# Optimization experiments

Measured on AMD Instinct MI355X. Metric: run time of the kernel, lower is better.

Reference implementation:

```python
import jax, jax.numpy as jnp
import numpy as np

B, T, D, N, R = 2, 2048, 1024, 16, 64  # batch, seqlen, d_model, d_state, dt_rank


def setup_inputs() -> dict:
    key = jax.random.key(0)
    ks = jax.random.split(key, 8)
    sc = 0.02  # init scale for weights
    return {
        "x": jax.random.normal(ks[0], (B, T, D), jnp.float32),
        "W_in": jax.random.normal(ks[1], (2 * D, D), jnp.float32) * sc,   # in_proj.weight
        "conv_w": jax.random.normal(ks[2], (D, 3), jnp.float32) * sc,     # conv1d.weight [D,1,3] squeezed
        "W_x": jax.random.normal(ks[3], (R + 2 * N, D), jnp.float32) * sc, # x_proj.weight
        "W_dt": jax.random.normal(ks[4], (D, R), jnp.float32) * sc,        # dt_proj.weight
        "b_dt": jnp.ones((D,), jnp.float32),                               # dt_proj.bias (init 1.0)
        "A_log": jnp.full((D, N), -2.0, jnp.float32),                      # A_log (filled -2.0)
        "D_param": jnp.ones((D,), jnp.float32),                            # D skip
        "W_C": jax.random.normal(ks[5], (D, N), jnp.float32) * sc,         # C_proj.weight
        "W_out": jax.random.normal(ks[6], (D, D), jnp.float32) * sc,       # out_proj.weight
    }


def reference(x, W_in, conv_w, W_x, W_dt, b_dt, A_log, D_param, W_C, W_out):
    # in_proj -> chunk into (x, z)
    xz = jnp.einsum('btd,ed->bte', x, W_in)           # [B,T,2D]
    xc, z = jnp.split(xz, 2, axis=-1)                 # [B,T,D] each

    # depthwise conv1d, kernel 3, padding 1, no bias
    xp = jnp.pad(xc, ((0, 0), (1, 1), (0, 0)))
    xconv = (xp[:, :-2] * conv_w[:, 0]
             + xp[:, 1:-1] * conv_w[:, 1]
             + xp[:, 2:] * conv_w[:, 2])              # [B,T,D]
    xs = jax.nn.silu(xconv)

    # x_proj -> split dt / B / C params
    x_dbl = jnp.einsum('btd,ed->bte', xs, W_x)        # [B,T,R+2N]
    dt_param = x_dbl[..., :R]
    Bp = x_dbl[..., R:R + N]                          # [B,T,N]
    Cp = x_dbl[..., R + N:]                           # [B,T,N]

    dt = jax.nn.softplus(dt_param @ W_dt.T + b_dt) + 1e-5  # [B,T,D]

    # discretization
    A_disc = jnp.exp(-jnp.exp(A_log)[None, None] * dt[..., None])  # [B,T,D,N]
    Bx = Bp[:, :, None, :] * dt[..., None] * xs[..., None]         # [B,T,D,N]
    C = Cp @ W_C.T                                                  # [B,T,D]

    # selective scan: s_t = A_t * s_{t-1} + B_t * x_t;  y_t = C_t * sum_n s_t
    def step(s, inp):
        A_t, Bx_t = inp
        s = A_t * s + Bx_t
        return s, s.sum(-1)                           # carry [B,D,N], out [B,D]

    s0 = jnp.zeros((x.shape[0], D, N), x.dtype)
    _, ssum = jax.lax.scan(step, s0,
                           (A_disc.transpose(1, 0, 2, 3), Bx.transpose(1, 0, 2, 3)))
    ssum = ssum.transpose(1, 0, 2)                    # [B,T,D]

    y = C * ssum + D_param * xs                       # [B,T,D]
    return jnp.einsum('btd,ed->bte', y, W_out) * jax.nn.silu(z)
```

## Files before the change

### kernel.cpp

```cpp
#include <hip/hip_runtime.h>

typedef unsigned short u16;
typedef __attribute__((ext_vector_type(4))) float f4;
typedef __attribute__((ext_vector_type(4))) unsigned short us4;
typedef __attribute__((ext_vector_type(8))) unsigned short us8;
typedef __attribute__((ext_vector_type(8))) short s8v;
typedef __attribute__((ext_vector_type(4))) float f32x4;
typedef __attribute__((ext_vector_type(4))) unsigned int u4v;

#define DEVI __device__ __forceinline__

DEVI u16 f2bf(float f) {
  unsigned u = __float_as_uint(f);
  u = (u + 0x7FFFu + ((u >> 16) & 1u)) >> 16;
  return (u16)u;
}
DEVI float bf2f(u16 v) { return __uint_as_float(((unsigned)v) << 16); }
DEVI float siluf(float x) { return x / (1.f + __expf(-x)); }

__global__ void k_cvt_all(const float* __restrict__ x, const float* __restrict__ w1,
                          const float* __restrict__ wo, const float* __restrict__ wdt,
                          const float* __restrict__ wx,
                          u16* __restrict__ xb, u16* __restrict__ w1b,
                          u16* __restrict__ wob, u16* __restrict__ wdtb,
                          u16* __restrict__ wxb) {
  const int blk = blockIdx.x;
  const int tid = threadIdx.x;
  if (blk >= 7232) {
    int i = (blk - 7232) * 256 + tid;
    int row = i >> 8;
    us4 o;
    if (row < 96) {
      f4 v = ((const f4*)wx)[i];
#pragma unroll
      for (int j = 0; j < 4; ++j) o[j] = f2bf(v[j]);
    } else {
      o[0] = 0; o[1] = 0; o[2] = 0; o[3] = 0;
    }
    ((us4*)wxb)[i] = o;
    return;
  }
  const float* src; u16* dst; int i;
  if (blk < 4096)      { src = x;   dst = xb;   i = blk * 256 + tid; }
  else if (blk < 6144) { src = w1;  dst = w1b;  i = (blk - 4096) * 256 + tid; }
  else if (blk < 7168) { src = wo;  dst = wob;  i = (blk - 6144) * 256 + tid; }
  else                 { src = wdt; dst = wdtb; i = (blk - 7168) * 256 + tid; }
  f4 v = ((const f4*)src)[i];
  us4 o;
#pragma unroll
  for (int j = 0; j < 4; ++j) o[j] = f2bf(v[j]);
  ((us4*)dst)[i] = o;
}

template <int EPI>
__global__ __launch_bounds__(512, 2)
void k_gemm_bt(const u16* __restrict__ A, int lda,
               const u16* __restrict__ B, int ldb,
               float* __restrict__ C, int ldc, int nvalid,
               int K, int kchunk, size_t zstride, int lognx,
               const float* __restrict__ bvec,
               const u16* __restrict__ zsrc,
               u16* __restrict__ ob1, u16* __restrict__ ob2) {
  __shared__ __align__(16) char smem[16384];
  u16* As = (u16*)smem;
  u16* Bs = (u16*)(smem + 8192);
  const int tid = threadIdx.x;
  const int wave = tid >> 6, lane = tid & 63;

  const int nwg = gridDim.x * gridDim.y;
  int bid = blockIdx.y * gridDim.x + blockIdx.x;
  {
    const int cpx = nwg >> 3;
    bid = (bid & 7) * cpx + (bid >> 3);
  }
  const int mBase = (bid >> lognx) << 7;
  const int nBase = (bid & ((1 << lognx) - 1)) << 7;
  const int kbeg = blockIdx.z * kchunk;
  int kend = kbeg + kchunk; if (kend > K) kend = K;
  C += (size_t)blockIdx.z * zstride;

  const int wr = wave >> 2, wc = wave & 3;
  const int row0 = tid >> 2, kg = tid & 3;

  const u16* Ag = A + (size_t)(mBase + row0) * lda + kg * 8;
  const u16* Bg = B + (size_t)(nBase + row0) * ldb + kg * 8;
  char* ldsA = (char*)As + wave * 1024;
  char* ldsB = (char*)Bs + wave * 1024;

  const int fr = lane & 15, fk = (lane >> 4) << 3;
  const int aoff = ((wr << 6) + fr) * 32 + fk;
  const int boff = ((wc << 5) + fr) * 32 + fk;

  f32x4 acc[4][2];
#pragma unroll
  for (int m = 0; m < 4; ++m)
#pragma unroll
    for (int n = 0; n < 2; ++n) acc[m][n] = {0.f, 0.f, 0.f, 0.f};

  for (int k0 = kbeg; k0 < kend; k0 += 32) {
    __syncthreads();
    __builtin_amdgcn_global_load_lds((const __attribute__((address_space(1))) void*)(Ag + k0),
                                     (__attribute__((address_space(3))) void*)(ldsA), 16, 0, 0);
    __builtin_amdgcn_global_load_lds((const __attribute__((address_space(1))) void*)(Bg + k0),
                                     (__attribute__((address_space(3))) void*)(ldsB), 16, 0, 0);
    __syncthreads();
    s8v av[4], bv[2];
#pragma unroll
    for (int m = 0; m < 4; ++m) av[m] = *(const s8v*)(As + aoff + (m << 9));
#pragma unroll
    for (int n = 0; n < 2; ++n) bv[n] = *(const s8v*)(Bs + boff + (n << 9));
#pragma unroll
    for (int m = 0; m < 4; ++m)
#pragma unroll
      for (int n = 0; n < 2; ++n)
        acc[m][n] = __builtin_amdgcn_mfma_f32_16x16x32_bf16(av[m], bv[n], acc[m][n], 0, 0, 0);
  }

  if (EPI == 2) {
    u16* ct = (u16*)smem;
    u16* dst = (nBase < 1024) ? ob1 : ob2;
    const int ncol = nBase & 1023;
    const int r16 = (lane >> 4) << 2;
#pragma unroll
    for (int m = 0; m < 4; ++m) {
      __syncthreads();
#pragma unroll
      for (int n = 0; n < 2; ++n)
#pragma unroll
        for (int j = 0; j < 4; ++j)
          ct[(wr * 16 + r16 + j) * 128 + (wc << 5) + (n << 4) + fr] = f2bf(acc[m][n][j]);
      __syncthreads();
      {
        const int tr = tid >> 4;
        const int colq = (tid & 15) << 3;
        const int grow = mBase + ((tr >> 4) << 6) + (m << 4) + (tr & 15);
        *(us8*)(dst + ((size_t)grow << 10) + ncol + colq) = *(const us8*)(ct + tr * 128 + colq);
      }
    }
    return;
  }

  const int crow0 = mBase + (wr << 6) + ((lane >> 4) << 2);
  const int ccol0 = nBase + (wc << 5) + (lane & 15);
#pragma unroll
  for (int m = 0; m < 4; ++m) {
#pragma unroll
    for (int n = 0; n < 2; ++n) {
      const int cc = ccol0 + (n << 4);
      if (cc < nvalid) {
#pragma unroll
        for (int j = 0; j < 4; ++j) {
          const int rr = crow0 + (m << 4) + j;
          float v = acc[m][n][j];
          if (EPI == 0) {
            C[(size_t)rr * ldc + cc] = v;
          } else if (EPI == 1) {
            v *= siluf(bf2f(zsrc[((size_t)rr << 10) + cc]));
            C[(size_t)rr * ldc + cc] = v;
          } else {
            float pre = v + bvec[cc];
            float dtv = (pre > 20.f ? pre : __logf(1.f + __expf(pre))) + 1e-5f;
            ob1[((size_t)rr << 10) + cc] = f2bf(dtv);
          }
        }
      }
    }
  }
}

__global__ void k_red4(const float* __restrict__ parts, float* __restrict__ xdbl,
                       u16* __restrict__ xdblb) {
  const int i = blockIdx.x * 256 + threadIdx.x;
  f4 s = ((const f4*)parts)[i];
#pragma unroll
  for (int z = 1; z < 4; ++z) {
    f4 v = ((const f4*)(parts + (size_t)z * 393216))[i];
#pragma unroll
    for (int j = 0; j < 4; ++j) s[j] += v[j];
  }
  ((f4*)xdbl)[i] = s;
  us4 o;
#pragma unroll
  for (int j = 0; j < 4; ++j) o[j] = f2bf(s[j]);
  ((us4*)xdblb)[i] = o;
}

__global__ void k_conv2(const u16* __restrict__ xcb, const float* __restrict__ conv_w,
                        u16* __restrict__ xsb) {
  const int b = blockIdx.x >> 8;
  const int t0 = (blockIdx.x & 255) << 3;
  const int d = threadIdx.x << 2;
  const u16* base = xcb + ((size_t)b * 2048 << 10) + d;
  const f4* cw = (const f4*)(conv_w + d * 3);
  f4 c0 = cw[0], c1 = cw[1], c2 = cw[2];
  const float w[12] = {c0[0], c0[1], c0[2], c0[3], c1[0], c1[1], c1[2], c1[3],
                       c2[0], c2[1], c2[2], c2[3]};
  const f4 zero = {0.f, 0.f, 0.f, 0.f};
  auto ld = [&](int t) -> f4 {
    us4 v = *(const us4*)(base + ((size_t)t << 10));
    f4 r;
#pragma unroll
    for (int j = 0; j < 4; ++j) r[j] = bf2f(v[j]);
    return r;
  };
  f4 prev = (t0 == 0) ? zero : ld(t0 - 1);
  f4 cur = ld(t0);
#pragma unroll
  for (int i = 0; i < 8; ++i) {
    const int t = t0 + i;
    f4 nxt = (t == 2047) ? zero : ld(t + 1);
    us4 xbv;
#pragma unroll
    for (int j = 0; j < 4; ++j) {
      float xc = prev[j] * w[j * 3] + cur[j] * w[j * 3 + 1] + nxt[j] * w[j * 3 + 2];
      xbv[j] = f2bf(siluf(xc));
    }
    *(us4*)(xsb + ((size_t)(b * 2048 + t) << 10) + d) = xbv;
    prev = cur; cur = nxt;
  }
}

__global__ void k_scanA(const u16* __restrict__ dtb, const u16* __restrict__ xsb,
                        const float* __restrict__ xdbl, const float* __restrict__ A_log,
                        unsigned* __restrict__ PS) {
  __shared__ float bxs[32][16];
  const int tid = threadIdx.x;
  const int d = (blockIdx.x << 8) + tid;
  const int c = blockIdx.y;
  const int b = blockIdx.z;
  const int btBase = (b << 11) + (c << 5);
  for (int i = tid; i < 512; i += 256) {
    bxs[i >> 4][i & 15] = xdbl[(size_t)(btBase + (i >> 4)) * 96 + 64 + (i & 15)];
  }
  float a[16];
  {
    const f4* al = (const f4*)(A_log + d * 16);
#pragma unroll
    for (int q = 0; q < 4; ++q) {
      f4 v = al[q];
#pragma unroll
      for (int j = 0; j < 4; ++j) a[q * 4 + j] = -__expf(v[j]);
    }
  }
  bool uni = true;
#pragma unroll
  for (int n = 1; n < 16; ++n) uni = uni && (a[n] == a[0]);
  __syncthreads();
  float P[16], S[16];
#pragma unroll
  for (int n = 0; n < 16; ++n) { P[n] = 1.f; S[n] = 0.f; }
  if (uni) {
    const float a0 = a[0];
    float Pu = 1.f;
    for (int tau = 0; tau < 32; ++tau) {
      const size_t bt = btBase + tau;
      const float dt = bf2f(dtb[(bt << 10) + d]);
      const float dx = dt * bf2f(xsb[(bt << 10) + d]);
      const float Av = __expf(a0 * dt);
      Pu *= Av;
#pragma unroll
      for (int n = 0; n < 16; ++n) S[n] = fmaf(Av, S[n], bxs[tau][n] * dx);
    }
#pragma unroll
    for (int n = 0; n < 16; ++n) P[n] = Pu;
  } else {
    for (int tau = 0; tau < 32; ++tau) {
      const size_t bt = btBase + tau;
      const float dt = bf2f(dtb[(bt << 10) + d]);
      const float dx = dt * bf2f(xsb[(bt << 10) + d]);
#pragma unroll
      for (int n = 0; n < 16; ++n) {
        const float Av = __expf(a[n] * dt);
        P[n] *= Av;
        S[n] = fmaf(Av, S[n], bxs[tau][n] * dx);
      }
    }
  }
  const size_t base = (size_t)(((b << 6) + c) * 1024 + d) << 4;
#pragma unroll
  for (int q = 0; q < 4; ++q) {
    u4v pk;
#pragma unroll
    for (int j = 0; j < 4; ++j) {
      pk[j] = (unsigned)f2bf(P[q * 4 + j]) | ((unsigned)f2bf(S[q * 4 + j]) << 16);
    }
    *(u4v*)(PS + base + q * 4) = pk;
  }
}

__global__ void k_scanB(const unsigned* __restrict__ PS, u16* __restrict__ SI) {
  const int i = (blockIdx.x << 8) + threadIdx.x;
  const int n = i & 15;
  const int dd = (i >> 4) & 1023;
  const int b = i >> 14;
  float s = 0.f;
  for (int c = 0; c < 64; ++c) {
    const size_t idx = ((size_t)(((b << 6) + c) * 1024 + dd) << 4) + n;
    const unsigned w = PS[idx];
    SI[idx] = f2bf(s);
    s = fmaf(bf2f((u16)(w & 0xFFFF)), s, bf2f((u16)(w >> 16)));
  }
}

__global__ void k_scanC(const u16* __restrict__ dtb, const u16* __restrict__ xsb,
                        const float* __restrict__ xdbl, const float* __restrict__ A_log,
                        const u16* __restrict__ SI, const float* __restrict__ W_C,
                        const float* __restrict__ D_param, u16* __restrict__ yb) {
  __shared__ float bxs[32][32];
  const int tid = threadIdx.x;
  const int d = (blockIdx.x << 8) + tid;
  const int c = blockIdx.y;
  const int b = blockIdx.z;
  const int btBase = (b << 11) + (c << 5);
  for (int i = tid; i < 1024; i += 256) {
    bxs[i >> 5][i & 31] = xdbl[(size_t)(btBase + (i >> 5)) * 96 + 64 + (i & 31)];
  }
  float a[16], wc[16];
  {
    const f4* al = (const f4*)(A_log + d * 16);
    const f4* wcp = (const f4*)(W_C + d * 16);
#pragma unroll
    for (int q = 0; q < 4; ++q) {
      f4 v = al[q], u = wcp[q];
#pragma unroll
      for (int j = 0; j < 4; ++j) { a[q * 4 + j] = -__expf(v[j]); wc[q * 4 + j] = u[j]; }
    }
  }
  bool uni = true;
#pragma unroll
  for (int n = 1; n < 16; ++n) uni = uni && (a[n] == a[0]);
  const float Dp = D_param[d];
  float s[16];
  const size_t base = (size_t)(((b << 6) + c) * 1024 + d) << 4;
#pragma unroll
  for (int q = 0; q < 4; ++q) {
    us4 v = *(const us4*)(SI + base + q * 4);
#pragma unroll
    for (int j = 0; j < 4; ++j) s[q * 4 + j] = bf2f(v[j]);
  }
  __syncthreads();
  if (uni) {
    const float a0 = a[0];
    for (int tau = 0; tau < 32; ++tau) {
      const size_t bt = btBase + tau;
      const float dt = bf2f(dtb[(bt << 10) + d]);
      const float xs = bf2f(xsb[(bt << 10) + d]);
      const float dx = dt * xs;
      const float Av = __expf(a0 * dt);
      float ssum = 0.f, cp = 0.f;
#pragma unroll
      for (int n = 0; n < 16; ++n) {
        s[n] = fmaf(Av, s[n], bxs[tau][n] * dx);
        ssum += s[n];
        cp = fmaf(bxs[tau][16 + n], wc[n], cp);
      }
      const float y = fmaf(cp, ssum, Dp * xs);
      yb[(bt << 10) + d] = f2bf(y);
    }
  } else {
    for (int tau = 0; tau < 32; ++tau) {
      const size_t bt = btBase + tau;
      const float dt = bf2f(dtb[(bt << 10) + d]);
      const float xs = bf2f(xsb[(bt << 10) + d]);
      const float dx = dt * xs;
      float ssum = 0.f, cp = 0.f;
#pragma unroll
      for (int n = 0; n < 16; ++n) {
        const float Av = __expf(a[n] * dt);
        s[n] = fmaf(Av, s[n], bxs[tau][n] * dx);
        ssum += s[n];
        cp = fmaf(bxs[tau][16 + n], wc[n], cp);
      }
      const float y = fmaf(cp, ssum, Dp * xs);
      yb[(bt << 10) + d] = f2bf(y);
    }
  }
}

extern "C" void kernel_launch(void* const* d_in, const int* in_sizes, int n_in,
                              void* d_out, int out_size, void* d_ws, size_t ws_size,
                              hipStream_t stream) {
  const float* x     = (const float*)d_in[0];
  const float* W_in  = (const float*)d_in[1];
  const float* convw = (const float*)d_in[2];
  const float* W_x   = (const float*)d_in[3];
  const float* W_dt  = (const float*)d_in[4];
  const float* b_dt  = (const float*)d_in[5];
  const float* A_log = (const float*)d_in[6];
  const float* D_par = (const float*)d_in[7];
  const float* W_C   = (const float*)d_in[8];
  const float* W_out = (const float*)d_in[9];
  float* out = (float*)d_out;
  (void)in_sizes; (void)n_in; (void)out_size; (void)ws_size;

  char* w = (char*)d_ws;
  auto take = [&](size_t bytes) { char* p = w; w += (bytes + 255) & ~(size_t)255; return p; };
  u16* xb     = (u16*)take(8388608);
  u16* w1b    = (u16*)take(4194304);
  u16* wxb    = (u16*)take(262144);
  u16* wob    = (u16*)take(2097152);
  u16* wdtb   = (u16*)take(131072);
  u16* xdblb  = (u16*)take(786432);
  u16* yb     = (u16*)take(8388608);
  u16* xsb    = (u16*)take(8388608);
  u16* xcb    = (u16*)take(8388608);
  u16* zb     = (u16*)take(8388608);
  u16* dtb    = (u16*)take(8388608);
  float* xdblp= (float*)take(6291456);
  float* xdbl = (float*)take(1572864);
  unsigned* PS= (unsigned*)take(8388608);
  u16* SI     = (u16*)take(4194304);

  k_cvt_all<<<7360, 256, 0, stream>>>(x, W_in, W_out, W_dt, W_x,
                                      xb, w1b, wob, wdtb, wxb);
  dim3 g1(16, 32, 1);
  k_gemm_bt<2><<<g1, 512, 0, stream>>>(xb, 1024, w1b, 1024, nullptr, 0, 2048,
                                       1024, 1024, 0, 4, nullptr, nullptr, xcb, zb);
  k_conv2<<<512, 256, 0, stream>>>(xcb, convw, xsb);
  dim3 g2(1, 32, 4);
  k_gemm_bt<0><<<g2, 512, 0, stream>>>(xsb, 1024, wxb, 1024, xdblp, 96, 96,
                                       1024, 256, 393216, 0, nullptr, nullptr, nullptr, nullptr);
  k_red4<<<384, 256, 0, stream>>>(xdblp, xdbl, xdblb);
  dim3 g4(8, 32, 1);
  k_gemm_bt<3><<<g4, 512, 0, stream>>>(xdblb, 96, wdtb, 64, nullptr, 0, 1024,
                                       64, 64, 0, 3, b_dt, nullptr, dtb, nullptr);
  dim3 gs(4, 64, 2);
  k_scanA<<<gs, 256, 0, stream>>>(dtb, xsb, xdbl, A_log, PS);
  k_scanB<<<128, 256, 0, stream>>>(PS, SI);
  k_scanC<<<gs, 256, 0, stream>>>(dtb, xsb, xdbl, A_log, SI, W_C, D_par, yb);
  dim3 g3(8, 32, 1);
  k_gemm_bt<1><<<g3, 512, 0, stream>>>(yb, 1024, wob, 1024, out, 1024, 1024,
                                       1024, 1024, 0, 3, nullptr, zb, nullptr, nullptr);
}
```

Measured before the change: 132.1 us.

## Double GEMM K-step, batch bf16 epilogue, store split-K partials in bf16

The GEMM kernel now stages 64 K-elements per barrier pair into a doubled 32KB LDS buffer and runs two MFMA sub-steps per iteration. This halves the number of __syncthreads and global_load_lds rounds. The in_proj epilogue writes the whole 128x128 bf16 tile to LDS once and stores it in four coalesced passes, instead of syncing twice per row group. The x_proj split-K partials are written as bf16 rather than fp32, which halves that traffic and the reduction reads, at some cost in precision.

New measurement: 124.2 us. 1.06x faster.

```diff
diff --git a/kernel.cpp b/kernel.cpp
--- a/kernel.cpp
+++ b/kernel.cpp
@@ -61,9 +61,7 @@
                const float* __restrict__ bvec,
                const u16* __restrict__ zsrc,
                u16* __restrict__ ob1, u16* __restrict__ ob2) {
-  __shared__ __align__(16) char smem[16384];
-  u16* As = (u16*)smem;
-  u16* Bs = (u16*)(smem + 8192);
+  __shared__ __align__(16) char smem[32768];
   const int tid = threadIdx.x;
   const int wave = tid >> 6, lane = tid & 63;
 
@@ -77,15 +75,20 @@
   const int nBase = (bid & ((1 << lognx) - 1)) << 7;
   const int kbeg = blockIdx.z * kchunk;
   int kend = kbeg + kchunk; if (kend > K) kend = K;
-  C += (size_t)blockIdx.z * zstride;
+  if (EPI == 4) ob1 += (size_t)blockIdx.z * zstride;
+  else          C   += (size_t)blockIdx.z * zstride;
 
   const int wr = wave >> 2, wc = wave & 3;
   const int row0 = tid >> 2, kg = tid & 3;
 
   const u16* Ag = A + (size_t)(mBase + row0) * lda + kg * 8;
   const u16* Bg = B + (size_t)(nBase + row0) * ldb + kg * 8;
-  char* ldsA = (char*)As + wave * 1024;
-  char* ldsB = (char*)Bs + wave * 1024;
+  char* ldsA0 = smem + wave * 1024;
+  char* ldsA1 = smem + 8192 + wave * 1024;
+  char* ldsB0 = smem + 16384 + wave * 1024;
+  char* ldsB1 = smem + 24576 + wave * 1024;
+  const u16* As = (const u16*)smem;
+  const u16* Bs = (const u16*)(smem + 16384);
 
   const int fr = lane & 15, fk = (lane >> 4) << 3;
   const int aoff = ((wr << 6) + fr) * 32 + fk;
@@ -97,45 +100,55 @@
 #pragma unroll
     for (int n = 0; n < 2; ++n) acc[m][n] = {0.f, 0.f, 0.f, 0.f};
 
-  for (int k0 = kbeg; k0 < kend; k0 += 32) {
+  for (int k0 = kbeg; k0 < kend; k0 += 64) {
     __syncthreads();
     __builtin_amdgcn_global_load_lds((const __attribute__((address_space(1))) void*)(Ag + k0),
-                                     (__attribute__((address_space(3))) void*)(ldsA), 16, 0, 0);
+                                     (__attribute__((address_space(3))) void*)(ldsA0), 16, 0, 0);
+    __builtin_amdgcn_global_load_lds((const __attribute__((address_space(1))) void*)(Ag + k0 + 32),
+                                     (__attribute__((address_space(3))) void*)(ldsA1), 16, 0, 0);
     __builtin_amdgcn_global_load_lds((const __attribute__((address_space(1))) void*)(Bg + k0),
-                                     (__attribute__((address_space(3))) void*)(ldsB), 16, 0, 0);
+                                     (__attribute__((address_space(3))) void*)(ldsB0), 16, 0, 0);
+    __builtin_amdgcn_global_load_lds((const __attribute__((address_space(1))) void*)(Bg + k0 + 32),
+                                     (__attribute__((address_space(3))) void*)(ldsB1), 16, 0, 0);
     __syncthreads();
-    s8v av[4], bv[2];
-#pragma unroll
-    for (int m = 0; m < 4; ++m) av[m] = *(const s8v*)(As + aoff + (m << 9));
-#pragma unroll
-    for (int n = 0; n < 2; ++n) bv[n] = *(const s8v*)(Bs + boff + (n << 9));
-#pragma unroll
-    for (int m = 0; m < 4; ++m)
-#pragma unroll
-      for (int n = 0; n < 2; ++n)
-        acc[m][n] = __builtin_amdgcn_mfma_f32_16x16x32_bf16(av[m], bv[n], acc[m][n], 0, 0, 0);
+#pragma unroll
+    for (int kk = 0; kk < 2; ++kk) {
+      const u16* Ap = As + (kk << 12);
+      const u16* Bp = Bs + (kk << 12);
+      s8v av[4], bv[2];
+#pragma unroll
+      for (int m = 0; m < 4; ++m) av[m] = *(const s8v*)(Ap + aoff + (m << 9));
+#pragma unroll
+      for (int n = 0; n < 2; ++n) bv[n] = *(const s8v*)(Bp + boff + (n << 9));
+#pragma unroll
+      for (int m = 0; m < 4; ++m)
+#pragma unroll
+        for (int n = 0; n < 2; ++n)
+          acc[m][n] = __builtin_amdgcn_mfma_f32_16x16x32_bf16(av[m], bv[n], acc[m][n], 0, 0, 0);
+    }
   }
 
   if (EPI == 2) {
     u16* ct = (u16*)smem;
+    const int r16 = (lane >> 4) << 2;
+    __syncthreads();
+#pragma unroll
+    for (int m = 0; m < 4; ++m)
+#pragma unroll
+      for (int n = 0; n < 2; ++n)
+#pragma unroll
+        for (int j = 0; j < 4; ++j)
+          ct[((wr << 6) + (m << 4) + r16 + j) * 128 + (wc << 5) + (n << 4) + fr] =
+              f2bf(acc[m][n][j]);
+    __syncthreads();
     u16* dst = (nBase < 1024) ? ob1 : ob2;
     const int ncol = nBase & 1023;
-    const int r16 = (lane >> 4) << 2;
-#pragma unroll
-    for (int m = 0; m < 4; ++m) {
-      __syncthreads();
-#pragma unroll
-      for (int n = 0; n < 2; ++n)
-#pragma unroll
-        for (int j = 0; j < 4; ++j)
-          ct[(wr * 16 + r16 + j) * 128 + (wc << 5) + (n << 4) + fr] = f2bf(acc[m][n][j]);
-      __syncthreads();
-      {
-        const int tr = tid >> 4;
-        const int colq = (tid & 15) << 3;
-        const int grow = mBase + ((tr >> 4) << 6) + (m << 4) + (tr & 15);
-        *(us8*)(dst + ((size_t)grow << 10) + ncol + colq) = *(const us8*)(ct + tr * 128 + colq);
-      }
+#pragma unroll
+    for (int it = 0; it < 4; ++it) {
+      const int s = it * 512 + tid;
+      const int tr = s >> 4, colq = (s & 15) << 3;
+      *(us8*)(dst + ((size_t)(mBase + tr) << 10) + ncol + colq) =
+          *(const us8*)(ct + tr * 128 + colq);
     }
     return;
   }
@@ -157,10 +170,12 @@
           } else if (EPI == 1) {
             v *= siluf(bf2f(zsrc[((size_t)rr << 10) + cc]));
             C[(size_t)rr * ldc + cc] = v;
-          } else {
+          } else if (EPI == 3) {
             float pre = v + bvec[cc];
             float dtv = (pre > 20.f ? pre : __logf(1.f + __expf(pre))) + 1e-5f;
             ob1[((size_t)rr << 10) + cc] = f2bf(dtv);
+          } else {
+            ob1[(size_t)rr * ldc + cc] = f2bf(v);
           }
         }
       }
@@ -168,15 +183,15 @@
   }
 }
 
-__global__ void k_red4(const float* __restrict__ parts, float* __restrict__ xdbl,
+__global__ void k_red4(const u16* __restrict__ parts, float* __restrict__ xdbl,
                        u16* __restrict__ xdblb) {
   const int i = blockIdx.x * 256 + threadIdx.x;
-  f4 s = ((const f4*)parts)[i];
-#pragma unroll
-  for (int z = 1; z < 4; ++z) {
-    f4 v = ((const f4*)(parts + (size_t)z * 393216))[i];
-#pragma unroll
-    for (int j = 0; j < 4; ++j) s[j] += v[j];
+  f4 s = {0.f, 0.f, 0.f, 0.f};
+#pragma unroll
+  for (int z = 0; z < 4; ++z) {
+    us4 v = ((const us4*)(parts + (size_t)z * 393216))[i];
+#pragma unroll
+    for (int j = 0; j < 4; ++j) s[j] += bf2f(v[j]);
   }
   ((f4*)xdbl)[i] = s;
   us4 o;
@@ -406,7 +421,7 @@
   u16* xcb    = (u16*)take(8388608);
   u16* zb     = (u16*)take(8388608);
   u16* dtb    = (u16*)take(8388608);
-  float* xdblp= (float*)take(6291456);
+  u16* xdblp  = (u16*)take(3145728);
   float* xdbl = (float*)take(1572864);
   unsigned* PS= (unsigned*)take(8388608);
   u16* SI     = (u16*)take(4194304);
@@ -418,8 +433,8 @@
                                        1024, 1024, 0, 4, nullptr, nullptr, xcb, zb);
   k_conv2<<<512, 256, 0, stream>>>(xcb, convw, xsb);
   dim3 g2(1, 32, 4);
-  k_gemm_bt<0><<<g2, 512, 0, stream>>>(xsb, 1024, wxb, 1024, xdblp, 96, 96,
-                                       1024, 256, 393216, 0, nullptr, nullptr, nullptr, nullptr);
+  k_gemm_bt<4><<<g2, 512, 0, stream>>>(xsb, 1024, wxb, 1024, nullptr, 96, 96,
+                                       1024, 256, 393216, 0, nullptr, nullptr, xdblp, nullptr);
   k_red4<<<384, 256, 0, stream>>>(xdblp, xdbl, xdblb);
   dim3 g4(8, 32, 1);
   k_gemm_bt<3><<<g4, 512, 0, stream>>>(xdblb, 96, wdtb, 64, nullptr, 0, 1024,
```
